# Kernel optimization log

Hardware: AMD Instinct MI355X
Metric: run time of the kernel (lower is better)

The kernel has to match this reference:

```python
import jax, jax.numpy as jnp
import numpy as np


def setup_inputs() -> dict:
    key = jax.random.key(0)
    k1, k2, k3 = jax.random.split(key, 3)
    B, q_len, c_len, D = 8, 512, 4096, 256  # D = 2*hidden_size
    q = jax.random.normal(k1, (B, q_len, D), dtype=jnp.float32)
    c = jax.random.normal(k2, (B, c_len, D), dtype=jnp.float32)
    # wsim: nn.Linear(3*D, 1, bias=False) -> weight vector of length 3*D
    w = jax.random.normal(k3, (3 * D,), dtype=jnp.float32) * (1.0 / np.sqrt(3 * D))
    return {"q": q, "c": c, "w": w}


def reference(q, c, w):
    # q: [B, q_len, D], c: [B, c_len, D], w: [3D] (concatenated [w_q, w_c, w_m])
    D = q.shape[-1]
    w_q, w_c, w_m = w[:D], w[D:2 * D], w[2 * D:]
    # S[b,i,j] = w . [q_j, c_i, q_j*c_i]  (decomposed trilinear score, no 6H blowup)
    S = (c @ w_c)[:, :, None] + (q @ w_q)[:, None, :] \
        + jnp.einsum('bid,bjd->bij', c * w_m, q)  # [B, c_len, q_len]
    # context2query: softmax over query dim, then attend over q
    context2query = jnp.einsum('bij,bjd->bid', jax.nn.softmax(S, axis=-1), q)
    # query2context: softmax over c of max-over-q scores, attend over c, broadcast to c_len
    b_attn = jax.nn.softmax(jnp.max(S, axis=2), axis=-1)  # [B, c_len]
    query2context = jnp.einsum('bi,bid->bd', b_attn, c)[:, None, :]  # [B, 1, D]
    query2context = jnp.broadcast_to(query2context, c.shape)  # repeat over c_len
    return jnp.concatenate(
        [c, context2query, c * context2query, c * query2context], axis=2
    )  # [B, c_len, 4D]
```

## Files before the change

kernel.cpp:

```cpp
#include <hip/hip_runtime.h>

#define BB 8
#define CL 4096
#define QL 512
#define DD 256

typedef unsigned short u16;
typedef float f32x4 __attribute__((ext_vector_type(4)));
typedef short s16x8 __attribute__((ext_vector_type(8)));

static __device__ __forceinline__ u16 f2bf(float x) {
  unsigned int u = __float_as_uint(x);
  u += 0x7FFFu + ((u >> 16) & 1u);
  return (u16)(u >> 16);
}

__global__ __launch_bounds__(256) void prep_q_k(
    const float* __restrict__ q, const float* __restrict__ w,
    u16* __restrict__ qbf, u16* __restrict__ qTbf, float* __restrict__ qw_g)
{
  __shared__ u16 qs[8][256];
  __shared__ float red[8][32];
  int blk = blockIdx.x;
  int b = blk & 7;
  int j0 = (blk >> 3) * 8;
  int t = threadIdx.x;
  int r = t >> 5;
  int cs = (t & 31) * 8;

  const float* qrow = q + ((size_t)(b * QL + j0 + r)) * DD + cs;
  float4 v0 = *(const float4*)(qrow);
  float4 v1 = *(const float4*)(qrow + 4);
  float4 w0 = *(const float4*)(w + cs);
  float4 w1 = *(const float4*)(w + cs + 4);
  float pw = v0.x*w0.x + v0.y*w0.y + v0.z*w0.z + v0.w*w0.w
           + v1.x*w1.x + v1.y*w1.y + v1.z*w1.z + v1.w*w1.w;

  union { u16 u[8]; uint4 v; } pk;
  pk.u[0]=f2bf(v0.x); pk.u[1]=f2bf(v0.y); pk.u[2]=f2bf(v0.z); pk.u[3]=f2bf(v0.w);
  pk.u[4]=f2bf(v1.x); pk.u[5]=f2bf(v1.y); pk.u[6]=f2bf(v1.z); pk.u[7]=f2bf(v1.w);

  *(uint4*)(qbf + ((size_t)(b * QL + j0 + r)) * DD + cs) = pk.v;
  *(uint4*)(&qs[r][cs]) = pk.v;
  red[r][t & 31] = pw;
  __syncthreads();

  if (t < 8) {
    float s = 0.f;
    #pragma unroll
    for (int k = 0; k < 32; ++k) s += red[t][k];
    qw_g[b * QL + j0 + t] = s;
  }

  int d = t;
  union { u16 u[8]; uint4 v; } tp;
  #pragma unroll
  for (int jj = 0; jj < 8; ++jj) tp.u[jj] = qs[jj][d];
  *(uint4*)(qTbf + ((size_t)(b * DD + d)) * QL + j0) = tp.v;
}

__global__ __launch_bounds__(512, 4) void attn_main_k(
    const float* __restrict__ c, const float* __restrict__ w,
    const u16* __restrict__ qbf, const u16* __restrict__ qTbf,
    const float* __restrict__ qw_g,
    float* __restrict__ pm_g, float* __restrict__ z_g,
    float* __restrict__ part_g, float* __restrict__ out)
{
  __shared__ u16 pool[64 * 512];
  __shared__ float qw_s[QL];
  __shared__ float cw_s[64];
  __shared__ float red_m[64][8];
  __shared__ float red_z[64][8];
  __shared__ float invz_s[64];
  __shared__ float wgt_s[64];

  int t = threadIdx.x;
  int blk = blockIdx.x;
  int b = blk & 7;
  int tile = blk >> 3;
  int it0 = tile * 64;

  {
    int r = t >> 3;
    int cg = (t & 7) * 32;
    int swz = (r & 7) << 3;
    const float* crow = c + ((size_t)(b * CL + it0 + r)) * DD + cg;
    float* outrow = out + ((size_t)(b * CL + it0 + r)) * (4 * DD) + cg;
    float pcw = 0.f;
    #pragma unroll
    for (int u = 0; u < 32; u += 4) {
      f32x4 cv  = *(const f32x4*)(crow + u);
      f32x4 wcv = *(const f32x4*)(w + DD + cg + u);
      f32x4 wmv = *(const f32x4*)(w + 2 * DD + cg + u);
      *(f32x4*)(outrow + u) = cv;
      pcw += cv[0]*wcv[0] + cv[1]*wcv[1] + cv[2]*wcv[2] + cv[3]*wcv[3];
      ushort4 hv;
      hv.x = f2bf(cv[0] * wmv[0]); hv.y = f2bf(cv[1] * wmv[1]);
      hv.z = f2bf(cv[2] * wmv[2]); hv.w = f2bf(cv[3] * wmv[3]);
      *(ushort4*)(&pool[r * 256 + ((cg + u) ^ swz)]) = hv;
    }
    pcw += __shfl_xor(pcw, 1);
    pcw += __shfl_xor(pcw, 2);
    pcw += __shfl_xor(pcw, 4);
    if ((t & 7) == 0) cw_s[r] = pcw;
    qw_s[t] = qw_g[b * QL + t];
  }
  __syncthreads();

  int wv = t >> 6;
  int ln = t & 63;
  int lr = ln & 15;
  int lg = ln >> 4;
  int jc = wv * 64;
  int aswz = (lr & 7) << 3;

  f32x4 acc[4][4];
  #pragma unroll
  for (int m = 0; m < 4; ++m)
    #pragma unroll
    for (int n = 0; n < 4; ++n) acc[m][n] = (f32x4){0.f, 0.f, 0.f, 0.f};

  const u16* qb = qbf + (size_t)b * QL * DD + (size_t)(jc + lr) * DD + lg * 8;
  s16x8 bqn[4];
  #pragma unroll
  for (int n = 0; n < 4; ++n) bqn[n] = *(const s16x8*)(qb + (size_t)(n * 16) * DD);
  #pragma unroll
  for (int kk = 0; kk < 8; ++kk) {
    s16x8 bqc[4];
    #pragma unroll
    for (int n = 0; n < 4; ++n) bqc[n] = bqn[n];
    if (kk < 7) {
      #pragma unroll
      for (int n = 0; n < 4; ++n)
        bqn[n] = *(const s16x8*)(qb + (size_t)(n * 16) * DD + (kk + 1) * 32);
    }
    s16x8 a[4];
    #pragma unroll
    for (int m = 0; m < 4; ++m)
      a[m] = *(const s16x8*)(&pool[(m * 16 + lr) * 256 + ((kk * 32 + lg * 8) ^ aswz)]);
    #pragma unroll
    for (int m = 0; m < 4; ++m)
      #pragma unroll
      for (int n = 0; n < 4; ++n)
        acc[m][n] = __builtin_amdgcn_mfma_f32_16x16x32_bf16(a[m], bqc[n], acc[m][n], 0, 0, 0);
  }

  float qwv[4];
  #pragma unroll
  for (int n = 0; n < 4; ++n) qwv[n] = qw_s[jc + n * 16 + lr];

  #pragma unroll
  for (int m = 0; m < 4; ++m) {
    #pragma unroll
    for (int rr = 0; rr < 4; ++rr) {
      int row = m * 16 + lg * 4 + rr;
      float cwv = cw_s[row];
      float mx = -1e30f;
      #pragma unroll
      for (int n = 0; n < 4; ++n) {
        float s = acc[m][n][rr] + cwv + qwv[n];
        acc[m][n][rr] = s;
        mx = fmaxf(mx, s);
      }
      mx = fmaxf(mx, __shfl_xor(mx, 1));
      mx = fmaxf(mx, __shfl_xor(mx, 2));
      mx = fmaxf(mx, __shfl_xor(mx, 4));
      mx = fmaxf(mx, __shfl_xor(mx, 8));
      if (lr == 0) red_m[row][wv] = mx;
    }
  }
  __syncthreads();

  #pragma unroll
  for (int m = 0; m < 4; ++m) {
    #pragma unroll
    for (int rr = 0; rr < 4; ++rr) {
      int row = m * 16 + lg * 4 + rr;
      float4 m0 = *(const float4*)(&red_m[row][0]);
      float4 m1 = *(const float4*)(&red_m[row][4]);
      float mr = fmaxf(fmaxf(fmaxf(m0.x, m0.y), fmaxf(m0.z, m0.w)),
                       fmaxf(fmaxf(m1.x, m1.y), fmaxf(m1.z, m1.w)));
      int pswz = (row & 7) << 3;
      float s = 0.f;
      #pragma unroll
      for (int n = 0; n < 4; ++n) {
        float e = __expf(acc[m][n][rr] - mr);
        pool[row * 512 + ((jc + n * 16 + lr) ^ pswz)] = f2bf(e);
        s += e;
      }
      s += __shfl_xor(s, 1);
      s += __shfl_xor(s, 2);
      s += __shfl_xor(s, 4);
      s += __shfl_xor(s, 8);
      if (lr == 0) red_z[row][wv] = s;
    }
  }
  __syncthreads();

  if (wv == 0) {
    int row = ln;
    float4 m0 = *(const float4*)(&red_m[row][0]);
    float4 m1 = *(const float4*)(&red_m[row][4]);
    float mr = fmaxf(fmaxf(fmaxf(m0.x, m0.y), fmaxf(m0.z, m0.w)),
                     fmaxf(fmaxf(m1.x, m1.y), fmaxf(m1.z, m1.w)));
    float4 z0 = *(const float4*)(&red_z[row][0]);
    float4 z1 = *(const float4*)(&red_z[row][4]);
    float z = z0.x + z0.y + z0.z + z0.w + z1.x + z1.y + z1.z + z1.w;
    invz_s[row] = 1.0f / z;
    float pmx = mr;
    #pragma unroll
    for (int o = 1; o < 64; o <<= 1) pmx = fmaxf(pmx, __shfl_xor(pmx, o));
    float wg = __expf(mr - pmx);
    wgt_s[row] = wg;
    float zs = wg;
    #pragma unroll
    for (int o = 1; o < 64; o <<= 1) zs += __shfl_xor(zs, o);
    if (ln == 0) { pm_g[b * 64 + tile] = pmx; z_g[b * 64 + tile] = zs; }
  }

  f32x4 o2[4][2];
  #pragma unroll
  for (int m = 0; m < 4; ++m)
    #pragma unroll
    for (int n = 0; n < 2; ++n) o2[m][n] = (f32x4){0.f, 0.f, 0.f, 0.f};

  int dc = wv * 32;
  const u16* qtb = qTbf + (size_t)b * DD * QL + (size_t)(dc + lr) * QL + lg * 8;
  s16x8 bvn[2];
  #pragma unroll
  for (int n = 0; n < 2; ++n) bvn[n] = *(const s16x8*)(qtb + (size_t)(n * 16) * QL);
  #pragma unroll 4
  for (int kk = 0; kk < 16; ++kk) {
    s16x8 bvc[2];
    #pragma unroll
    for (int n = 0; n < 2; ++n) bvc[n] = bvn[n];
    if (kk < 15) {
      #pragma unroll
      for (int n = 0; n < 2; ++n)
        bvn[n] = *(const s16x8*)(qtb + (size_t)(n * 16) * QL + (kk + 1) * 32);
    }
    s16x8 pa[4];
    #pragma unroll
    for (int m = 0; m < 4; ++m)
      pa[m] = *(const s16x8*)(&pool[(m * 16 + lr) * 512 + ((kk * 32 + lg * 8) ^ aswz)]);
    #pragma unroll
    for (int m = 0; m < 4; ++m)
      #pragma unroll
      for (int n = 0; n < 2; ++n)
        o2[m][n] = __builtin_amdgcn_mfma_f32_16x16x32_bf16(bvc[n], pa[m], o2[m][n], 0, 0, 0);
  }
  __syncthreads();

  f32x4 psum[2];
  psum[0] = (f32x4){0.f, 0.f, 0.f, 0.f};
  psum[1] = (f32x4){0.f, 0.f, 0.f, 0.f};
  const float* cb = c + ((size_t)(b * CL + it0)) * DD;
  float* ob = out + ((size_t)(b * CL + it0)) * (4 * DD);
  #pragma unroll
  for (int n = 0; n < 2; ++n) {
    int d4 = dc + n * 16 + lg * 4;
    #pragma unroll
    for (int m = 0; m < 4; ++m) {
      int i = m * 16 + lr;
      f32x4 cv = *(const f32x4*)(cb + (size_t)i * DD + d4);
      f32x4 c2q = o2[m][n] * invz_s[i];
      *(f32x4*)(ob + (size_t)i * (4 * DD) + DD + d4) = c2q;
      *(f32x4*)(ob + (size_t)i * (4 * DD) + 2 * DD + d4) = cv * c2q;
      psum[n] += wgt_s[i] * cv;
    }
    #pragma unroll
    for (int j = 0; j < 4; ++j) {
      psum[n][j] += __shfl_xor(psum[n][j], 1);
      psum[n][j] += __shfl_xor(psum[n][j], 2);
      psum[n][j] += __shfl_xor(psum[n][j], 4);
      psum[n][j] += __shfl_xor(psum[n][j], 8);
    }
    if (lr == 0)
      *(f32x4*)(part_g + ((size_t)(b * 64 + tile)) * DD + d4) = psum[n];
  }
}

__global__ __launch_bounds__(256) void q2c_seg3_k(
    const float* __restrict__ c,
    const float* __restrict__ pm_g, const float* __restrict__ z_g,
    const float* __restrict__ part_g, float* __restrict__ out)
{
  __shared__ float wk[64];
  int blk = blockIdx.x;
  int b = blk & 7;
  int chunk = blk >> 3;
  int t = threadIdx.x;

  if (t < 64) {
    float p = pm_g[b * 64 + t];
    float m = p;
    #pragma unroll
    for (int o = 1; o < 64; o <<= 1) m = fmaxf(m, __shfl_xor(m, o));
    float ew = __expf(p - m);
    float zi = ew * z_g[b * 64 + t];
    float s = zi;
    #pragma unroll
    for (int o = 1; o < 64; o <<= 1) s += __shfl_xor(s, o);
    wk[t] = ew / s;
  }
  __syncthreads();

  int c4 = (t & 63) * 4;
  f32x4 g = (f32x4){0.f, 0.f, 0.f, 0.f};
  #pragma unroll 8
  for (int k = 0; k < 64; ++k)
    g += wk[k] * *(const f32x4*)(part_g + ((size_t)(b * 64 + k)) * DD + c4);

  int r0 = chunk * 128 + (t >> 6);
  for (int it = 0; it < 32; ++it) {
    int row = r0 + it * 4;
    f32x4 cv = *(const f32x4*)(c + ((size_t)(b * CL + row)) * DD + c4);
    *(f32x4*)(out + ((size_t)(b * CL + row)) * (4 * DD) + 3 * DD + c4) = cv * g;
  }
}

extern "C" void kernel_launch(void* const* d_in, const int* in_sizes, int n_in,
                              void* d_out, int out_size, void* d_ws, size_t ws_size,
                              hipStream_t stream) {
  const float* q = (const float*)d_in[0];
  const float* c = (const float*)d_in[1];
  const float* w = (const float*)d_in[2];
  float* out = (float*)d_out;
  char* ws = (char*)d_ws;

  u16*   qbf   = (u16*)(ws);
  u16*   qTbf  = (u16*)(ws + 2097152);
  float* qw    = (float*)(ws + 4194304);
  float* pm    = (float*)(ws + 4210688);
  float* zb    = (float*)(ws + 4214784);
  float* part  = (float*)(ws + 4218880);

  prep_q_k<<<512, 256, 0, stream>>>(q, w, qbf, qTbf, qw);
  attn_main_k<<<512, 512, 0, stream>>>(c, w, qbf, qTbf, qw, pm, zb, part, out);
  q2c_seg3_k<<<256, 256, 0, stream>>>(c, pm, zb, part, out);
}
```

Measured before the change: 94.60 us.

## Halve attention row tile, fuse softmax passes, and move c copy to epilogue

Shrinks the per-block context tile from 64 to 32 rows, doubling the grid to 1024 blocks and raising the launch-bounds occupancy hint to 6. Splits LDS into separate c*w_m and probability buffers, so shared memory per block drops. Drops the max-subtraction before exp so max and sum are reduced in one pass with one fewer barrier; the per-row c·w_c term is added back only for the query-to-context max. The copy of c into the output moves into the epilogue, and the q2c kernel now merges 128 partials per batch. The tradeoffs are overflow risk in exp for large scores, more partials to combine, and the loss of register prefetching of q fragments.

```diff
diff --git a/kernel.cpp b/kernel.cpp
--- a/kernel.cpp
+++ b/kernel.cpp
@@ -59,53 +59,25 @@
   *(uint4*)(qTbf + ((size_t)(b * DD + d)) * QL + j0) = tp.v;
 }
 
-__global__ __launch_bounds__(512, 4) void attn_main_k(
+__global__ __launch_bounds__(512, 6) void attn_main_k(
     const float* __restrict__ c, const float* __restrict__ w,
     const u16* __restrict__ qbf, const u16* __restrict__ qTbf,
     const float* __restrict__ qw_g,
     float* __restrict__ pm_g, float* __restrict__ z_g,
     float* __restrict__ part_g, float* __restrict__ out)
 {
-  __shared__ u16 pool[64 * 512];
+  __shared__ u16 cm[32 * 256];
+  __shared__ u16 P[32 * 512];
   __shared__ float qw_s[QL];
-  __shared__ float cw_s[64];
-  __shared__ float red_m[64][8];
-  __shared__ float red_z[64][8];
-  __shared__ float invz_s[64];
-  __shared__ float wgt_s[64];
+  __shared__ float cw_s[32];
+  __shared__ float red_m[32][8];
+  __shared__ float red_z[32][8];
 
   int t = threadIdx.x;
   int blk = blockIdx.x;
   int b = blk & 7;
   int tile = blk >> 3;
-  int it0 = tile * 64;
-
-  {
-    int r = t >> 3;
-    int cg = (t & 7) * 32;
-    int swz = (r & 7) << 3;
-    const float* crow = c + ((size_t)(b * CL + it0 + r)) * DD + cg;
-    float* outrow = out + ((size_t)(b * CL + it0 + r)) * (4 * DD) + cg;
-    float pcw = 0.f;
-    #pragma unroll
-    for (int u = 0; u < 32; u += 4) {
-      f32x4 cv  = *(const f32x4*)(crow + u);
-      f32x4 wcv = *(const f32x4*)(w + DD + cg + u);
-      f32x4 wmv = *(const f32x4*)(w + 2 * DD + cg + u);
-      *(f32x4*)(outrow + u) = cv;
-      pcw += cv[0]*wcv[0] + cv[1]*wcv[1] + cv[2]*wcv[2] + cv[3]*wcv[3];
-      ushort4 hv;
-      hv.x = f2bf(cv[0] * wmv[0]); hv.y = f2bf(cv[1] * wmv[1]);
-      hv.z = f2bf(cv[2] * wmv[2]); hv.w = f2bf(cv[3] * wmv[3]);
-      *(ushort4*)(&pool[r * 256 + ((cg + u) ^ swz)]) = hv;
-    }
-    pcw += __shfl_xor(pcw, 1);
-    pcw += __shfl_xor(pcw, 2);
-    pcw += __shfl_xor(pcw, 4);
-    if ((t & 7) == 0) cw_s[r] = pcw;
-    qw_s[t] = qw_g[b * QL + t];
-  }
-  __syncthreads();
+  int it0 = tile * 32;
 
   int wv = t >> 6;
   int ln = t & 63;
@@ -114,35 +86,54 @@
   int jc = wv * 64;
   int aswz = (lr & 7) << 3;
 
-  f32x4 acc[4][4];
-  #pragma unroll
-  for (int m = 0; m < 4; ++m)
+  {
+    int r = t >> 4;
+    int cq = (t & 15) * 16;
+    int swz = (r & 7) << 3;
+    const float* crow = c + ((size_t)(b * CL + it0 + r)) * DD + cq;
+    float pcw = 0.f;
+    #pragma unroll
+    for (int u = 0; u < 16; u += 4) {
+      f32x4 cv  = *(const f32x4*)(crow + u);
+      f32x4 wcv = *(const f32x4*)(w + DD + cq + u);
+      f32x4 wmv = *(const f32x4*)(w + 2 * DD + cq + u);
+      pcw += cv[0]*wcv[0] + cv[1]*wcv[1] + cv[2]*wcv[2] + cv[3]*wcv[3];
+      ushort4 hv;
+      hv.x = f2bf(cv[0] * wmv[0]); hv.y = f2bf(cv[1] * wmv[1]);
+      hv.z = f2bf(cv[2] * wmv[2]); hv.w = f2bf(cv[3] * wmv[3]);
+      *(ushort4*)(&cm[r * 256 + ((cq + u) ^ swz)]) = hv;
+    }
+    pcw += __shfl_xor(pcw, 1);
+    pcw += __shfl_xor(pcw, 2);
+    pcw += __shfl_xor(pcw, 4);
+    pcw += __shfl_xor(pcw, 8);
+    if ((t & 15) == 0) cw_s[r] = pcw;
+    qw_s[t] = qw_g[b * QL + t];
+  }
+  __syncthreads();
+
+  f32x4 acc[2][4];
+  #pragma unroll
+  for (int m = 0; m < 2; ++m)
     #pragma unroll
     for (int n = 0; n < 4; ++n) acc[m][n] = (f32x4){0.f, 0.f, 0.f, 0.f};
 
   const u16* qb = qbf + (size_t)b * QL * DD + (size_t)(jc + lr) * DD + lg * 8;
-  s16x8 bqn[4];
-  #pragma unroll
-  for (int n = 0; n < 4; ++n) bqn[n] = *(const s16x8*)(qb + (size_t)(n * 16) * DD);
   #pragma unroll
   for (int kk = 0; kk < 8; ++kk) {
-    s16x8 bqc[4];
-    #pragma unroll
-    for (int n = 0; n < 4; ++n) bqc[n] = bqn[n];
-    if (kk < 7) {
+    s16x8 bq[4];
+    #pragma unroll
+    for (int n = 0; n < 4; ++n)
+      bq[n] = *(const s16x8*)(qb + (size_t)(n * 16) * DD + kk * 32);
+    s16x8 a[2];
+    #pragma unroll
+    for (int m = 0; m < 2; ++m)
+      a[m] = *(const s16x8*)(&cm[(m * 16 + lr) * 256 + ((kk * 32 + lg * 8) ^ aswz)]);
+    #pragma unroll
+    for (int m = 0; m < 2; ++m)
       #pragma unroll
       for (int n = 0; n < 4; ++n)
-        bqn[n] = *(const s16x8*)(qb + (size_t)(n * 16) * DD + (kk + 1) * 32);
-    }
-    s16x8 a[4];
-    #pragma unroll
-    for (int m = 0; m < 4; ++m)
-      a[m] = *(const s16x8*)(&pool[(m * 16 + lr) * 256 + ((kk * 32 + lg * 8) ^ aswz)]);
-    #pragma unroll
-    for (int m = 0; m < 4; ++m)
-      #pragma unroll
-      for (int n = 0; n < 4; ++n)
-        acc[m][n] = __builtin_amdgcn_mfma_f32_16x16x32_bf16(a[m], bqc[n], acc[m][n], 0, 0, 0);
+        acc[m][n] = __builtin_amdgcn_mfma_f32_16x16x32_bf16(a[m], bq[n], acc[m][n], 0, 0, 0);
   }
 
   float qwv[4];
@@ -150,133 +141,111 @@
   for (int n = 0; n < 4; ++n) qwv[n] = qw_s[jc + n * 16 + lr];
 
   #pragma unroll
-  for (int m = 0; m < 4; ++m) {
+  for (int m = 0; m < 2; ++m) {
     #pragma unroll
     for (int rr = 0; rr < 4; ++rr) {
       int row = m * 16 + lg * 4 + rr;
-      float cwv = cw_s[row];
+      int pswz = (row & 7) << 3;
       float mx = -1e30f;
+      float s = 0.f;
       #pragma unroll
       for (int n = 0; n < 4; ++n) {
-        float s = acc[m][n][rr] + cwv + qwv[n];
-        acc[m][n][rr] = s;
-        mx = fmaxf(mx, s);
+        float sv = acc[m][n][rr] + qwv[n];
+        mx = fmaxf(mx, sv);
+        float e = __expf(sv);
+        s += e;
+        P[row * 512 + ((jc + n * 16 + lr) ^ pswz)] = f2bf(e);
       }
       mx = fmaxf(mx, __shfl_xor(mx, 1));
       mx = fmaxf(mx, __shfl_xor(mx, 2));
       mx = fmaxf(mx, __shfl_xor(mx, 4));
       mx = fmaxf(mx, __shfl_xor(mx, 8));
-      if (lr == 0) red_m[row][wv] = mx;
-    }
-  }
-  __syncthreads();
-
-  #pragma unroll
-  for (int m = 0; m < 4; ++m) {
-    #pragma unroll
-    for (int rr = 0; rr < 4; ++rr) {
-      int row = m * 16 + lg * 4 + rr;
-      float4 m0 = *(const float4*)(&red_m[row][0]);
-      float4 m1 = *(const float4*)(&red_m[row][4]);
-      float mr = fmaxf(fmaxf(fmaxf(m0.x, m0.y), fmaxf(m0.z, m0.w)),
-                       fmaxf(fmaxf(m1.x, m1.y), fmaxf(m1.z, m1.w)));
-      int pswz = (row & 7) << 3;
-      float s = 0.f;
-      #pragma unroll
-      for (int n = 0; n < 4; ++n) {
-        float e = __expf(acc[m][n][rr] - mr);
-        pool[row * 512 + ((jc + n * 16 + lr) ^ pswz)] = f2bf(e);
-        s += e;
-      }
       s += __shfl_xor(s, 1);
       s += __shfl_xor(s, 2);
       s += __shfl_xor(s, 4);
       s += __shfl_xor(s, 8);
-      if (lr == 0) red_z[row][wv] = s;
+      if (lr == 0) { red_m[row][wv] = mx; red_z[row][wv] = s; }
     }
   }
   __syncthreads();
 
-  if (wv == 0) {
-    int row = ln;
-    float4 m0 = *(const float4*)(&red_m[row][0]);
-    float4 m1 = *(const float4*)(&red_m[row][4]);
-    float mr = fmaxf(fmaxf(fmaxf(m0.x, m0.y), fmaxf(m0.z, m0.w)),
-                     fmaxf(fmaxf(m1.x, m1.y), fmaxf(m1.z, m1.w)));
-    float4 z0 = *(const float4*)(&red_z[row][0]);
-    float4 z1 = *(const float4*)(&red_z[row][4]);
-    float z = z0.x + z0.y + z0.z + z0.w + z1.x + z1.y + z1.z + z1.w;
-    invz_s[row] = 1.0f / z;
-    float pmx = mr;
-    #pragma unroll
-    for (int o = 1; o < 64; o <<= 1) pmx = fmaxf(pmx, __shfl_xor(pmx, o));
-    float wg = __expf(mr - pmx);
-    wgt_s[row] = wg;
-    float zs = wg;
-    #pragma unroll
-    for (int o = 1; o < 64; o <<= 1) zs += __shfl_xor(zs, o);
-    if (ln == 0) { pm_g[b * 64 + tile] = pmx; z_g[b * 64 + tile] = zs; }
-  }
-
-  f32x4 o2[4][2];
-  #pragma unroll
-  for (int m = 0; m < 4; ++m)
+  f32x4 o2[2][2];
+  #pragma unroll
+  for (int m = 0; m < 2; ++m)
     #pragma unroll
     for (int n = 0; n < 2; ++n) o2[m][n] = (f32x4){0.f, 0.f, 0.f, 0.f};
 
   int dc = wv * 32;
   const u16* qtb = qTbf + (size_t)b * DD * QL + (size_t)(dc + lr) * QL + lg * 8;
-  s16x8 bvn[2];
-  #pragma unroll
-  for (int n = 0; n < 2; ++n) bvn[n] = *(const s16x8*)(qtb + (size_t)(n * 16) * QL);
-  #pragma unroll 4
+  #pragma unroll
   for (int kk = 0; kk < 16; ++kk) {
-    s16x8 bvc[2];
-    #pragma unroll
-    for (int n = 0; n < 2; ++n) bvc[n] = bvn[n];
-    if (kk < 15) {
+    s16x8 bv[2];
+    #pragma unroll
+    for (int n = 0; n < 2; ++n)
+      bv[n] = *(const s16x8*)(qtb + (size_t)(n * 16) * QL + kk * 32);
+    s16x8 pa[2];
+    #pragma unroll
+    for (int m = 0; m < 2; ++m)
+      pa[m] = *(const s16x8*)(&P[(m * 16 + lr) * 512 + ((kk * 32 + lg * 8) ^ aswz)]);
+    #pragma unroll
+    for (int m = 0; m < 2; ++m)
       #pragma unroll
       for (int n = 0; n < 2; ++n)
-        bvn[n] = *(const s16x8*)(qtb + (size_t)(n * 16) * QL + (kk + 1) * 32);
-    }
-    s16x8 pa[4];
-    #pragma unroll
-    for (int m = 0; m < 4; ++m)
-      pa[m] = *(const s16x8*)(&pool[(m * 16 + lr) * 512 + ((kk * 32 + lg * 8) ^ aswz)]);
-    #pragma unroll
-    for (int m = 0; m < 4; ++m)
-      #pragma unroll
-      for (int n = 0; n < 2; ++n)
-        o2[m][n] = __builtin_amdgcn_mfma_f32_16x16x32_bf16(bvc[n], pa[m], o2[m][n], 0, 0, 0);
-  }
-  __syncthreads();
-
-  f32x4 psum[2];
-  psum[0] = (f32x4){0.f, 0.f, 0.f, 0.f};
-  psum[1] = (f32x4){0.f, 0.f, 0.f, 0.f};
+        o2[m][n] = __builtin_amdgcn_mfma_f32_16x16x32_bf16(bv[n], pa[m], o2[m][n], 0, 0, 0);
+  }
+
+  float invz[2], wgt[2], mtrue[2];
+  #pragma unroll
+  for (int m = 0; m < 2; ++m) {
+    int i = m * 16 + lr;
+    float4 m0 = *(const float4*)(&red_m[i][0]);
+    float4 m1 = *(const float4*)(&red_m[i][4]);
+    mtrue[m] = cw_s[i] + fmaxf(fmaxf(fmaxf(m0.x, m0.y), fmaxf(m0.z, m0.w)),
+                               fmaxf(fmaxf(m1.x, m1.y), fmaxf(m1.z, m1.w)));
+    float4 z0 = *(const float4*)(&red_z[i][0]);
+    float4 z1 = *(const float4*)(&red_z[i][4]);
+    invz[m] = 1.0f / (z0.x + z0.y + z0.z + z0.w + z1.x + z1.y + z1.z + z1.w);
+  }
+  float pmx = fmaxf(mtrue[0], mtrue[1]);
+  pmx = fmaxf(pmx, __shfl_xor(pmx, 1));
+  pmx = fmaxf(pmx, __shfl_xor(pmx, 2));
+  pmx = fmaxf(pmx, __shfl_xor(pmx, 4));
+  pmx = fmaxf(pmx, __shfl_xor(pmx, 8));
+  wgt[0] = __expf(mtrue[0] - pmx);
+  wgt[1] = __expf(mtrue[1] - pmx);
+  float zs = wgt[0] + wgt[1];
+  zs += __shfl_xor(zs, 1);
+  zs += __shfl_xor(zs, 2);
+  zs += __shfl_xor(zs, 4);
+  zs += __shfl_xor(zs, 8);
+  if (wv == 0 && ln == 0) { pm_g[b * 128 + tile] = pmx; z_g[b * 128 + tile] = zs; }
+
   const float* cb = c + ((size_t)(b * CL + it0)) * DD;
   float* ob = out + ((size_t)(b * CL + it0)) * (4 * DD);
   #pragma unroll
   for (int n = 0; n < 2; ++n) {
     int d4 = dc + n * 16 + lg * 4;
-    #pragma unroll
-    for (int m = 0; m < 4; ++m) {
+    f32x4 psum = (f32x4){0.f, 0.f, 0.f, 0.f};
+    #pragma unroll
+    for (int m = 0; m < 2; ++m) {
       int i = m * 16 + lr;
       f32x4 cv = *(const f32x4*)(cb + (size_t)i * DD + d4);
-      f32x4 c2q = o2[m][n] * invz_s[i];
-      *(f32x4*)(ob + (size_t)i * (4 * DD) + DD + d4) = c2q;
-      *(f32x4*)(ob + (size_t)i * (4 * DD) + 2 * DD + d4) = cv * c2q;
-      psum[n] += wgt_s[i] * cv;
+      f32x4 c2q = o2[m][n] * invz[m];
+      float* orow = ob + (size_t)i * (4 * DD);
+      *(f32x4*)(orow + d4) = cv;
+      *(f32x4*)(orow + DD + d4) = c2q;
+      *(f32x4*)(orow + 2 * DD + d4) = cv * c2q;
+      psum += wgt[m] * cv;
     }
     #pragma unroll
     for (int j = 0; j < 4; ++j) {
-      psum[n][j] += __shfl_xor(psum[n][j], 1);
-      psum[n][j] += __shfl_xor(psum[n][j], 2);
-      psum[n][j] += __shfl_xor(psum[n][j], 4);
-      psum[n][j] += __shfl_xor(psum[n][j], 8);
+      psum[j] += __shfl_xor(psum[j], 1);
+      psum[j] += __shfl_xor(psum[j], 2);
+      psum[j] += __shfl_xor(psum[j], 4);
+      psum[j] += __shfl_xor(psum[j], 8);
     }
     if (lr == 0)
-      *(f32x4*)(part_g + ((size_t)(b * 64 + tile)) * DD + d4) = psum[n];
+      *(f32x4*)(part_g + ((size_t)(b * 128 + tile)) * DD + d4) = psum;
   }
 }
 
@@ -285,31 +254,41 @@
     const float* __restrict__ pm_g, const float* __restrict__ z_g,
     const float* __restrict__ part_g, float* __restrict__ out)
 {
-  __shared__ float wk[64];
+  __shared__ float wk[128];
+  __shared__ float rm[2];
+  __shared__ float rz[2];
   int blk = blockIdx.x;
   int b = blk & 7;
   int chunk = blk >> 3;
   int t = threadIdx.x;
 
-  if (t < 64) {
-    float p = pm_g[b * 64 + t];
+  float p = (t < 128) ? pm_g[b * 128 + t] : -1e30f;
+  if (t < 128) {
     float m = p;
     #pragma unroll
     for (int o = 1; o < 64; o <<= 1) m = fmaxf(m, __shfl_xor(m, o));
-    float ew = __expf(p - m);
-    float zi = ew * z_g[b * 64 + t];
+    if ((t & 63) == 0) rm[t >> 6] = m;
+  }
+  __syncthreads();
+  float M = fmaxf(rm[0], rm[1]);
+  if (t < 128) {
+    float ew = __expf(p - M);
+    float zi = ew * z_g[b * 128 + t];
     float s = zi;
     #pragma unroll
     for (int o = 1; o < 64; o <<= 1) s += __shfl_xor(s, o);
-    wk[t] = ew / s;
-  }
-  __syncthreads();
+    if ((t & 63) == 0) rz[t >> 6] = s;
+    wk[t] = ew;
+  }
+  __syncthreads();
+  float Zinv = 1.0f / (rz[0] + rz[1]);
 
   int c4 = (t & 63) * 4;
   f32x4 g = (f32x4){0.f, 0.f, 0.f, 0.f};
   #pragma unroll 8
-  for (int k = 0; k < 64; ++k)
-    g += wk[k] * *(const f32x4*)(part_g + ((size_t)(b * 64 + k)) * DD + c4);
+  for (int k = 0; k < 128; ++k)
+    g += wk[k] * *(const f32x4*)(part_g + ((size_t)(b * 128 + k)) * DD + c4);
+  g *= Zinv;
 
   int r0 = chunk * 128 + (t >> 6);
   for (int it = 0; it < 32; ++it) {
@@ -336,6 +315,6 @@
   float* part  = (float*)(ws + 4218880);
 
   prep_q_k<<<512, 256, 0, stream>>>(q, w, qbf, qTbf, qw);
-  attn_main_k<<<512, 512, 0, stream>>>(c, w, qbf, qTbf, qw, pm, zb, part, out);
+  attn_main_k<<<1024, 512, 0, stream>>>(c, w, qbf, qTbf, qw, pm, zb, part, out);
   q2c_seg3_k<<<256, 256, 0, stream>>>(c, pm, zb, part, out);
 }
```

After: 111.5 us. +17.8%, slower.
